# Performance work log

Measured on AMD Instinct MI355X. Metric: run time of the kernel, lower is better.

## Reference

```python
import jax, jax.numpy as jnp
import numpy as np

N = 512    # nnodes
H = 8      # attention heads
C = 32     # gnn_repr_size (per head)
ER = 32    # edge_repr_size
FE = 3     # feat_emb_size
E = 16384  # edges (avg degree 32)


def gat_conv(x, edge_index, edge_attr, W, att_src, att_dst, We, att_edge, b):
    """PyG GATConv (edge_dim=1, concat=True, add_self_loops=True, eval mode)."""
    n = x.shape[0]
    h_, c_ = att_src.shape
    row, col = edge_index[0], edge_index[1]
    # self loops with fill_value='mean': mean of incoming edge_attr per target node
    deg = jax.ops.segment_sum(jnp.ones_like(edge_attr), col, num_segments=n)
    loop_attr = jax.ops.segment_sum(edge_attr, col, num_segments=n) / jnp.maximum(deg, 1.0)
    ar = jnp.arange(n)
    row = jnp.concatenate([row, ar])
    col = jnp.concatenate([col, ar])
    ea = jnp.concatenate([edge_attr, loop_attr])
    # node projections [n, H, C]
    h = (x @ W.T).reshape(n, h_, c_)
    a_src = jnp.sum(h * att_src, axis=-1)  # [n, H]
    a_dst = jnp.sum(h * att_dst, axis=-1)  # [n, H]
    e = (ea[:, None] @ We.T).reshape(-1, h_, c_)  # [E', H, C]
    a_e = jnp.sum(e * att_edge, axis=-1)          # [E', H]
    alpha = jax.nn.leaky_relu(a_src[row] + a_dst[col] + a_e, 0.2)
    # softmax over edges grouped by destination node
    amax = jax.ops.segment_max(alpha, col, num_segments=n)
    ex = jnp.exp(alpha - amax[col])
    denom = jax.ops.segment_sum(ex, col, num_segments=n)
    alpha = ex / (denom[col] + 1e-16)
    out = jax.ops.segment_sum(h[row] * alpha[..., None], col, num_segments=n)
    return out.reshape(n, h_ * c_) + b


def setup_inputs():
    key = jax.random.key(0)
    ks = jax.random.split(key, 24)
    s = 0.05
    HC = H * C
    in_len = N * ER + 3 * N + 3 * FE  # combiner1 input length
    return {
        "dist": jax.random.uniform(ks[0], (N, N), dtype=jnp.float32),
        "markov": jax.random.uniform(ks[1], (N, N), dtype=jnp.float32),
        "demand": jax.random.normal(ks[2], (N,), dtype=jnp.float32),
        "W_week": jax.random.normal(ks[3], (7, FE)) * s,
        "W_cap": jax.random.normal(ks[4], (26, FE)) * s,
        "W_veh": jax.random.normal(ks[5], (15, FE)) * s,
        "g1_W": jax.random.normal(ks[6], (HC, 1)) * s,
        "g1_att_src": jax.random.normal(ks[7], (H, C)) * s,
        "g1_att_dst": jax.random.normal(ks[8], (H, C)) * s,
        "g1_We": jax.random.normal(ks[9], (HC, 1)) * s,
        "g1_att_edge": jax.random.normal(ks[10], (H, C)) * s,
        "g1_b": jnp.zeros((HC,), dtype=jnp.float32),
        "g2_W": jax.random.normal(ks[11], (HC, HC)) * s,
        "g2_att_src": jax.random.normal(ks[12], (H, C)) * s,
        "g2_att_dst": jax.random.normal(ks[13], (H, C)) * s,
        "g2_We": jax.random.normal(ks[14], (HC, 1)) * s,
        "g2_att_edge": jax.random.normal(ks[15], (H, C)) * s,
        "g2_b": jnp.zeros((HC,), dtype=jnp.float32),
        "Wes": jax.random.normal(ks[16], (ER, 2 * HC)) * s,
        "bes": jnp.zeros((ER,), dtype=jnp.float32),
        "Wc1": jax.random.normal(ks[17], (N, in_len)) * 0.01,
        "bc1": jnp.zeros((N,), dtype=jnp.float32),
        "Wc2": jax.random.normal(ks[18], (N, N)) * s,
        "bc2": jnp.zeros((N,), dtype=jnp.float32),
        "stops": jax.random.randint(ks[19], (256,), 0, N),
        "edge_index": jax.random.randint(ks[20], (2, E), 0, N),
        "weekday": 3,
        "vehicles": 7,
        "capacity": 12,
    }


def reference(dist, markov, demand, W_week, W_cap, W_veh,
              g1_W, g1_att_src, g1_att_dst, g1_We, g1_att_edge, g1_b,
              g2_W, g2_att_src, g2_att_dst, g2_We, g2_att_edge, g2_b,
              Wes, bes, Wc1, bc1, Wc2, bc2,
              stops, edge_index, weekday, vehicles, capacity):
    n = dist.shape[0]
    dist = (dist - dist.min()) / (dist.max() - dist.min())
    x = demand[:, None]  # [n, 1]
    ea = markov[edge_index[0], edge_index[1]]  # [E]
    x = jax.nn.relu(gat_conv(x, edge_index, ea, g1_W, g1_att_src, g1_att_dst, g1_We, g1_att_edge, g1_b))
    x = jax.nn.relu(gat_conv(x, edge_index, ea, g2_W, g2_att_src, g2_att_dst, g2_We, g2_att_edge, g2_b))
    HC_ = x.shape[1]
    # all-pairs edge representation: concat(x[i], x[j]) over meshgrid -> [n*n, 2*HC]
    er = jnp.concatenate([
        jnp.broadcast_to(x[:, None, :], (n, n, HC_)),
        jnp.broadcast_to(x[None, :, :], (n, n, HC_)),
    ], axis=-1).reshape(n * n, 2 * HC_)
    er = (er @ Wes.T + bes).reshape(n, -1)  # [n, n*ER]
    week = jnp.broadcast_to(W_week[weekday], (n, W_week.shape[1]))
    cap = jnp.broadcast_to(W_cap[capacity], (n, W_cap.shape[1]))
    veh = jnp.broadcast_to(W_veh[vehicles], (n, W_veh.shape[1]))
    stop = jnp.broadcast_to(jnp.zeros((n,), dtype=dist.dtype).at[stops].set(1.0)[None, :], (n, n))
    feat = jnp.concatenate([er, dist, markov, week, cap, veh, stop], axis=1)
    out = jax.nn.relu(feat @ Wc1.T + bc1) @ Wc2.T + bc2
    return out
```

## Files before the change

### kernel.cpp

```cpp
#include <hip/hip_runtime.h>
#include <hip/hip_bf16.h>

typedef __hip_bfloat16 bf16;
typedef __attribute__((ext_vector_type(8))) short bf16x8;
typedef __attribute__((ext_vector_type(4))) float f32x4;

#define NNODE 512
#define NEDGE 16384
#define INLEN 17929
#define K1    1056

#define WS_EA      0
#define WS_CSRC    16384
#define WS_CEA     32768
#define WS_DEG     49152
#define WS_STARTS  49664
#define WS_LATTR   50176
#define WS_MM      50688
#define WS_MMP     50690
#define WS_STOPV   50818
#define WS_AE      51330
#define WS_PS      51346
#define WS_H       55552
#define WS_G2WT    186624
#define WS_H2      317696
#define WS_ASRC    448768
#define WS_ADST    452864
#define WS_UV      456960
#define WS_K       489728
#define WS_APACK   490240
#define WS_BPACK   760576
#define WS_OUT1    1030912
#define WS_WC2B    1161984
#define WS_WESF    1293056
#define WS_ASRC2   1309440
#define WS_ADST2   1313536
#define WS_CURSOR  1317632
#define WS_DEGP    1318144
#define WS_LSUMP   1350912

__global__ __launch_bounds__(256)
void k_prep(const float* __restrict__ demand, const float* __restrict__ W1,
            const float* __restrict__ att_s, const float* __restrict__ att_d,
            const int* __restrict__ stops, const float* __restrict__ Wes,
            const float* __restrict__ dist, const float* __restrict__ markov,
            const int* __restrict__ eidx,
            const float* __restrict__ g1We, const float* __restrict__ g1ae,
            const float* __restrict__ g2We, const float* __restrict__ g2ae,
            const float* __restrict__ g2W,  const float* __restrict__ g2as,
            const float* __restrict__ g2ad, float* ws){
  int b = blockIdx.x, tid = threadIdx.x;
  if (b < 512){
    int hd = tid>>5, c = tid&31;
    float hv = demand[b] * W1[tid];
    ws[WS_H + b*256 + tid] = hv;
    float ps = hv * att_s[tid];
    float pd = hv * att_d[tid];
    for (int off=16; off; off>>=1){ ps += __shfl_down(ps,off,32); pd += __shfl_down(pd,off,32); }
    if (c==0){ ws[WS_ASRC + b*8+hd]=ps; ws[WS_ADST + b*8+hd]=pd; }
  } else if (b == 512){
    ws[WS_STOPV+tid] = 0.f; ws[WS_STOPV+256+tid] = 0.f;
    __syncthreads();
    ws[WS_STOPV + stops[tid]] = 1.0f;
    if (tid < 8){
      float s=0.f; for (int c=0;c<32;c++) s += g1We[tid*32+c]*g1ae[tid*32+c];
      ws[WS_AE+tid]=s;
    } else if (tid < 16){
      int h=tid-8; float s=0.f; for (int c=0;c<32;c++) s += g2We[h*32+c]*g2ae[h*32+c];
      ws[WS_AE+8+h]=s;
    }
  } else if (b < 515){
    for (int idx = (b-513)*8192 + tid; idx < (b-512)*8192; idx += 256){
      int k = idx>>8, c = idx&255;
      ws[WS_WESF+idx] = (k<32) ? Wes[k*512+c] : Wes[(k-32)*512+256+c];
    }
  } else if (b < 579){
    __shared__ float smn[256], smx[256];
    int p = b-515;
    float mn = 3.4e38f, mx = -3.4e38f;
    const float4* dv = (const float4*)(dist + p*4096);
    #pragma unroll
    for (int k=0;k<4;k++){
      float4 v = dv[k*256 + tid];
      mn = fminf(mn, fminf(fminf(v.x,v.y), fminf(v.z,v.w)));
      mx = fmaxf(mx, fmaxf(fmaxf(v.x,v.y), fmaxf(v.z,v.w)));
    }
    smn[tid]=mn; smx[tid]=mx; __syncthreads();
    for (int off=128; off; off>>=1){
      if (tid<off){ smn[tid]=fminf(smn[tid],smn[tid+off]); smx[tid]=fmaxf(smx[tid],smx[tid+off]); }
      __syncthreads();
    }
    if (tid==0){ ws[WS_MMP+p]=smn[0]; ws[WS_MMP+64+p]=smx[0]; }
  } else if (b < 643){
    __shared__ int   hd_[512];
    __shared__ float hf_[512];
    int k = b-579;
    hd_[tid]=0; hd_[256+tid]=0; hf_[tid]=0.f; hf_[256+tid]=0.f;
    __syncthreads();
    int e = k*256 + tid;
    int r = eidx[e], c = eidx[NEDGE+e];
    float a = markov[r*NNODE + c];
    ws[WS_EA+e] = a;
    atomicAdd(&hd_[c], 1);
    atomicAdd(&hf_[c], a);
    __syncthreads();
    ((int*)(ws+WS_DEGP))[k*512+tid]     = hd_[tid];
    ((int*)(ws+WS_DEGP))[k*512+256+tid] = hd_[256+tid];
    ws[WS_LSUMP + k*512+tid]     = hf_[tid];
    ws[WS_LSUMP + k*512+256+tid] = hf_[256+tid];
  } else if (b < 659){
    int j = b-643;
    const float* att = (j<8) ? g2as : g2ad;
    int h = j&7;
    float s = 0.f;
    for (int c=0;c<32;c++) s += att[h*32+c] * g2W[(h*32+c)*256 + tid];
    ws[WS_PS + j*256 + tid] = s;
  } else if (b < 675){
    __shared__ float T[64][65];
    int tb = b-659, tr = tb>>2, tc = tb&3;
    int w = tid>>6, c = tid&63;
    for (int k=0;k<16;k++){
      int r = k*4 + w;
      T[r][c] = g2W[(tr*64+r)*256 + tc*64 + c];
    }
    __syncthreads();
    for (int k=0;k<16;k++){
      int r = k*4 + w;
      ws[WS_G2WT + (tc*64+r)*256 + tr*64 + c] = T[c][r];
    }
  } else {
    ((int*)(ws+WS_CURSOR))[tid] = 0;
    ((int*)(ws+WS_CURSOR))[256+tid] = 0;
  }
}

__global__ __launch_bounds__(512)
void k_scansc(const int* __restrict__ eidx, float* ws){
  __shared__ int sc[512];
  __shared__ int startS[512];
  __shared__ float rmn[64], rmx[64];
  int t = threadIdx.x, b = blockIdx.x;
  const int* dp = (const int*)(ws+WS_DEGP);
  int d = 0;
  for (int k=0;k<64;k++) d += dp[k*512+t];
  sc[t] = d; __syncthreads();
  for (int off=1; off<512; off<<=1){
    int v = (t>=off) ? sc[t-off] : 0; __syncthreads();
    sc[t] += v; __syncthreads();
  }
  startS[t] = sc[t]-d;
  if (b == 0){
    float l = 0.f;
    for (int k=0;k<64;k++) l += ws[WS_LSUMP+k*512+t];
    ((int*)(ws+WS_STARTS))[t] = startS[t];
    ((int*)(ws+WS_DEG))[t] = d;
    ws[WS_LATTR+t] = l / (float)(d>1 ? d : 1);
    if (t < 64){ rmn[t]=ws[WS_MMP+t]; rmx[t]=ws[WS_MMP+64+t]; }
    __syncthreads();
    if (t == 0){
      float mn=rmn[0], mx=rmx[0];
      for (int i=1;i<64;i++){ mn=fminf(mn,rmn[i]); mx=fmaxf(mx,rmx[i]); }
      ws[WS_MM]=mn; ws[WS_MM+1]=mx;
    }
  }
  __syncthreads();
  int e = b*512 + t;
  int c = eidx[NEDGE+e];
  int p = startS[c] + atomicAdd((int*)(ws+WS_CURSOR)+c, 1);
  ((int*)(ws+WS_CSRC))[p] = eidx[e];
  ws[WS_CEA+p] = ws[WS_EA+e];
}

template<int MODE>
__global__ __launch_bounds__(256)
void k_agg(const float* __restrict__ hbuf, const float* __restrict__ asrc,
           const float* __restrict__ adst, const int* __restrict__ csrc,
           const float* __restrict__ cea, const int* __restrict__ starts,
           const int* __restrict__ deg, const float* __restrict__ lattr,
           const float* __restrict__ AEp, const float* __restrict__ bvec,
           const float* __restrict__ dist, const float* __restrict__ markov,
           float* ws){
  int t = blockIdx.x, tid = threadIdx.x, hd = tid>>5;
  __shared__ int   srcE[256];
  __shared__ float eaE[256];
  __shared__ float Lall[256*8];
  __shared__ float AE[8], mh[8], dh[8], sw[8];
  __shared__ float xrow[256], uvrow[64];
  if (tid<8) AE[tid]=AEp[tid];
  __syncthreads();
  int d = deg[t], s0 = starts[t];
  if (d > 256) d = 256;
  for (int e=tid; e<d; e+=256){ srcE[e]=csrc[s0+e]; eaE[e]=cea[s0+e]; }
  __syncthreads();
  {
    int h8 = tid&7;
    float adt = adst[t*8+h8], aeh = AE[h8];
    for (int e = tid>>3; e < d; e += 32){
      float a = asrc[srcE[e]*8+h8] + adt + eaE[e]*aeh;
      Lall[e*8+h8] = a>=0.f ? a : 0.2f*a;
    }
  }
  __syncthreads();
  {
    int h = tid>>5, j = tid&31;
    float aself = asrc[t*8+h] + adst[t*8+h] + lattr[t]*AE[h];
    aself = aself>=0.f ? aself : 0.2f*aself;
    float mm = aself;
    for (int e=j; e<d; e+=32) mm = fmaxf(mm, Lall[e*8+h]);
    for (int off=16; off; off>>=1) mm = fmaxf(mm, __shfl_down(mm,off,32));
    mm = __shfl(mm, 0, 32);
    float dd = 0.f;
    for (int e=j; e<d; e+=32) dd += __expf(Lall[e*8+h]-mm);
    for (int off=16; off; off>>=1) dd += __shfl_down(dd,off,32);
    if (j==0){
      float se = __expf(aself-mm);
      mh[h]=mm; dh[h]=dd+se+1e-16f; sw[h]=se;
    }
  }
  __syncthreads();
  {
    int h8 = tid&7;
    for (int e = tid>>3; e < d; e += 32)
      Lall[e*8+h8] = __expf(Lall[e*8+h8] - mh[h8]);
  }
  __syncthreads();
  float a0 = sw[hd]*hbuf[t*256+tid], a1=0.f, a2=0.f, a3=0.f;
  int e = 0;
  for (; e+4<=d; e+=4){
    a0 += Lall[(e+0)*8+hd]*hbuf[srcE[e+0]*256+tid];
    a1 += Lall[(e+1)*8+hd]*hbuf[srcE[e+1]*256+tid];
    a2 += Lall[(e+2)*8+hd]*hbuf[srcE[e+2]*256+tid];
    a3 += Lall[(e+3)*8+hd]*hbuf[srcE[e+3]*256+tid];
  }
  for (; e<d; e++) a0 += Lall[e*8+hd]*hbuf[srcE[e]*256+tid];
  float v = fmaxf(((a0+a1)+(a2+a3))/dh[hd] + bvec[tid], 0.f);
  xrow[tid] = v;
  __syncthreads();
  if (MODE == 1){
    const float* g2wt = ws + WS_G2WT;
    float h0=0.f,h1=0.f,h2=0.f,h3=0.f;
    for (int c=0;c<256;c+=4){
      h0 += xrow[c+0]*g2wt[(c+0)*256+tid];
      h1 += xrow[c+1]*g2wt[(c+1)*256+tid];
      h2 += xrow[c+2]*g2wt[(c+2)*256+tid];
      h3 += xrow[c+3]*g2wt[(c+3)*256+tid];
    }
    ws[WS_H2 + t*256 + tid] = (h0+h1)+(h2+h3);
    if (tid < 64){
      int j = tid>>2, q = tid&3;
      const float* pr = ws + WS_PS + j*256 + q*64;
      const float* xr = xrow + q*64;
      float p = 0.f;
      for (int c=0;c<64;c++) p += xr[c]*pr[c];
      p += __shfl_down(p,2,4);
      p += __shfl_down(p,1,4);
      if (q==0){
        if (j<8) ws[WS_ASRC2 + t*8+j] = p;
        else     ws[WS_ADST2 + t*8+(j-8)] = p;
      }
    }
  } else {
    int k = tid>>2, q = tid&3;
    const float* wr = ws + WS_WESF + k*256 + q*64;
    const float* xr = xrow + q*64;
    float p = 0.f;
    for (int c=0;c<64;c++) p += xr[c]*wr[c];
    p += __shfl_down(p,2,4);
    p += __shfl_down(p,1,4);
    if (q==0){ ws[WS_UV + t*64+k] = p; uvrow[k] = p; }
    __syncthreads();
    float mn = ws[WS_MM], mx = ws[WS_MM+1];
    float inv = 1.0f/(mx-mn);
    bf16* ap = (bf16*)(ws+WS_APACK);
    const float* mrow = markov + t*512;
    for (int j=tid; j<K1; j+=256){
      float v2;
      if (j<32)       v2 = uvrow[j];
      else if (j<544) v2 = (dist[t*512 + j-32] - mn) * inv;
      else            v2 = mrow[j-544];
      ap[(size_t)t*K1 + j] = __float2bfloat16(v2);
    }
  }
}

__global__ __launch_bounds__(1024)
void k_skpack(const float* __restrict__ Wc1, const float* __restrict__ bc1,
              const float* __restrict__ bes, const float* __restrict__ Wweek,
              const float* __restrict__ Wcap, const float* __restrict__ Wveh,
              const int* __restrict__ wd, const int* __restrict__ vh,
              const int* __restrict__ cp, const float* __restrict__ Wc2,
              float* ws){
  int o = blockIdx.x, tid = threadIdx.x;
  __shared__ float besf[32];
  __shared__ float red[1024];
  if (tid<32) besf[tid] = bes[tid];
  __syncthreads();
  const float* wr = Wc1 + (size_t)o*INLEN;
  bf16* bp  = (bf16*)(ws+WS_BPACK);
  bf16* w2b = (bf16*)(ws+WS_WC2B);
  float be = besf[tid&31];
  const float* uvp = ws + WS_UV + ((tid>>5)<<6) + 32 + (tid&31);
  float sP = 0.f, tP0=0.f, tP1=0.f, tP2=0.f, tP3=0.f;
  #pragma unroll
  for (int i=0;i<16;i+=4){
    float w0 = wr[tid + 1024*(i+0)];
    float w1 = wr[tid + 1024*(i+1)];
    float w2 = wr[tid + 1024*(i+2)];
    float w3 = wr[tid + 1024*(i+3)];
    float u0 = uvp[2048*(i+0)];
    float u1 = uvp[2048*(i+1)];
    float u2 = uvp[2048*(i+2)];
    float u3 = uvp[2048*(i+3)];
    sP += (w0+w1)+(w2+w3);
    tP0 += w0*(u0+be);
    tP1 += w1*(u1+be);
    tP2 += w2*(u2+be);
    tP3 += w3*(u3+be);
  }
  float tP = (tP0+tP1)+(tP2+tP3);
  if (tid < 512) tP += ws[WS_STOPV+tid] * wr[17417+tid];
  if (tid < 9){
    int g = tid/3, f = tid-g*3;
    float sv = (g==0) ? Wweek[wd[0]*3+f]
             : (g==1) ? Wcap[cp[0]*3+f]
                      : Wveh[vh[0]*3+f];
    tP += sv * wr[17408+tid];
  }
  red[tid] = sP; __syncthreads();
  for (int off=512; off>=32; off>>=1){
    if (tid<off) red[tid] += red[tid+off];
    __syncthreads();
  }
  if (tid<32) bp[(size_t)o*K1 + tid] = __float2bfloat16(red[tid]);
  __syncthreads();
  red[tid] = tP; __syncthreads();
  for (int off=512; off; off>>=1){
    if (tid<off) red[tid] += red[tid+off];
    __syncthreads();
  }
  if (tid==0) ws[WS_K+o] = red[0] + bc1[o];
  bp[(size_t)o*K1 + 32 + tid] = __float2bfloat16(wr[16384+tid]);
  if (tid < 512) w2b[o*512+tid] = __float2bfloat16(Wc2[o*512+tid]);
}

template<bool RELU, bool BF16OUT>
__global__ __launch_bounds__(256)
void gemm_mfma(const bf16* __restrict__ A, const bf16* __restrict__ B,
               const float* __restrict__ bias, float* __restrict__ Cf,
               bf16* __restrict__ Cb, int M, int N, int K){
  __shared__ short Als[2][2048];
  __shared__ short Bls[2][2048];
  const int tid = threadIdx.x;
  const int bm = blockIdx.y*64, bn = blockIdx.x*64;
  const int wave = tid>>6, lane = tid&63;
  const int wm = wave>>1, wn = wave&1;
  const int r = lane&15, q = lane>>4;
  f32x4 acc[2][2] = {};
  const int lrow = tid>>2, lq = tid&3;
  const bf16* Ag = A + (size_t)(bm+lrow)*K + lq*8;
  const bf16* Bg = B + (size_t)(bn+lrow)*K + lq*8;
  const int sidx = (lq*64+lrow)*8;
  const int nk = K>>5;
  float4 av = *(const float4*)(Ag);
  float4 bv = *(const float4*)(Bg);
  *(float4*)(&Als[0][sidx]) = av;
  *(float4*)(&Bls[0][sidx]) = bv;
  __syncthreads();
  for (int kk=0; kk<nk; kk++){
    int cur = kk&1, nxt = cur^1;
    if (kk+1 < nk){
      av = *(const float4*)(Ag + (kk+1)*32);
      bv = *(const float4*)(Bg + (kk+1)*32);
    }
    #pragma unroll
    for (int i=0;i<2;i++){
      bf16x8 af = *(const bf16x8*)(&Als[cur][(q*64 + wm*32 + i*16 + r)*8]);
      #pragma unroll
      for (int j=0;j<2;j++){
        bf16x8 bfr = *(const bf16x8*)(&Bls[cur][(q*64 + wn*32 + j*16 + r)*8]);
        acc[i][j] = __builtin_amdgcn_mfma_f32_16x16x32_bf16(af, bfr, acc[i][j], 0,0,0);
      }
    }
    if (kk+1 < nk){
      __syncthreads();
      *(float4*)(&Als[nxt][sidx]) = av;
      *(float4*)(&Bls[nxt][sidx]) = bv;
      __syncthreads();
    }
  }
  #pragma unroll
  for (int i=0;i<2;i++){
    int row = bm + wm*32 + i*16 + q*4;
    #pragma unroll
    for (int j=0;j<2;j++){
      int col = bn + wn*32 + j*16 + r;
      float bi = bias ? bias[col] : 0.f;
      #pragma unroll
      for (int g=0; g<4; g++){
        float v = acc[i][j][g] + bi;
        if (RELU) v = fmaxf(v, 0.f);
        if (BF16OUT) Cb[(size_t)(row+g)*N + col] = __float2bfloat16(v);
        else         Cf[(size_t)(row+g)*N + col] = v;
      }
    }
  }
}

extern "C" void kernel_launch(void* const* d_in, const int* in_sizes, int n_in,
                              void* d_out, int out_size, void* d_ws, size_t ws_size,
                              hipStream_t stream){
  const float* dist   = (const float*)d_in[0];
  const float* markov = (const float*)d_in[1];
  const float* demand = (const float*)d_in[2];
  const float* Wweek  = (const float*)d_in[3];
  const float* Wcap   = (const float*)d_in[4];
  const float* Wveh   = (const float*)d_in[5];
  const float* g1W    = (const float*)d_in[6];
  const float* g1as   = (const float*)d_in[7];
  const float* g1ad   = (const float*)d_in[8];
  const float* g1We   = (const float*)d_in[9];
  const float* g1ae   = (const float*)d_in[10];
  const float* g1b    = (const float*)d_in[11];
  const float* g2W    = (const float*)d_in[12];
  const float* g2as   = (const float*)d_in[13];
  const float* g2ad   = (const float*)d_in[14];
  const float* g2We   = (const float*)d_in[15];
  const float* g2ae   = (const float*)d_in[16];
  const float* g2b    = (const float*)d_in[17];
  const float* Wes    = (const float*)d_in[18];
  const float* bes    = (const float*)d_in[19];
  const float* Wc1    = (const float*)d_in[20];
  const float* bc1    = (const float*)d_in[21];
  const float* Wc2    = (const float*)d_in[22];
  const float* bc2    = (const float*)d_in[23];
  const int*   stops  = (const int*)d_in[24];
  const int*   eidx   = (const int*)d_in[25];
  const int*   wd     = (const int*)d_in[26];
  const int*   vh     = (const int*)d_in[27];
  const int*   cp     = (const int*)d_in[28];
  float* out = (float*)d_out;
  float* ws = (float*)d_ws;

  const int*   csrc   = (const int*)(ws+WS_CSRC);
  const float* cea    = ws+WS_CEA;
  const int*   starts = (const int*)(ws+WS_STARTS);
  const int*   deg    = (const int*)(ws+WS_DEG);
  const float* lattr  = ws+WS_LATTR;

  k_prep<<<676,256,0,stream>>>(demand, g1W, g1as, g1ad, stops, Wes, dist, markov, eidx,
                               g1We, g1ae, g2We, g2ae, g2W, g2as, g2ad, ws);
  k_scansc<<<32,512,0,stream>>>(eidx, ws);
  k_agg<1><<<512,256,0,stream>>>(ws+WS_H, ws+WS_ASRC, ws+WS_ADST, csrc, cea, starts, deg,
                                 lattr, ws+WS_AE, g1b, dist, markov, ws);
  k_agg<2><<<512,256,0,stream>>>(ws+WS_H2, ws+WS_ASRC2, ws+WS_ADST2, csrc, cea, starts, deg,
                                 lattr, ws+WS_AE+8, g2b, dist, markov, ws);
  k_skpack<<<512,1024,0,stream>>>(Wc1, bc1, bes, Wweek, Wcap, Wveh, wd, vh, cp, Wc2, ws);
  gemm_mfma<true,true><<<dim3(8,8),256,0,stream>>>((const bf16*)(ws+WS_APACK), (const bf16*)(ws+WS_BPACK),
                                                   ws+WS_K, nullptr, (bf16*)(ws+WS_OUT1), 512, 512, K1);
  gemm_mfma<false,false><<<dim3(8,8),256,0,stream>>>((const bf16*)(ws+WS_OUT1), (const bf16*)(ws+WS_WC2B),
                                                     bc2, out, nullptr, 512, 512, 512);
}
```

Measured before the change: 204.8 us.

## Widen GEMM to 512 threads with K=64 steps, shuffle reductions, move Wc2 cast

The MFMA GEMM now runs 8 waves per 64x64 tile with a 64-wide K step, so each wave owns a 32x16 output and there are half as many barriers per K. To fit the wider step, the first GEMM's K is zero-padded from 1056 to 1088. The k_skpack reductions switch from shared-memory trees with many barriers to wave shuffles plus a small final pass. The Wc2 bf16 conversion moves into extra k_prep blocks using vectorised loads and stores. The trade-off is more shared memory per block and some padded zero work.

```diff
diff --git a/kernel.cpp b/kernel.cpp
--- a/kernel.cpp
+++ b/kernel.cpp
@@ -8,7 +8,7 @@
 #define NNODE 512
 #define NEDGE 16384
 #define INLEN 17929
-#define K1    1056
+#define K1P   1088
 
 #define WS_EA      0
 #define WS_CSRC    16384
@@ -29,15 +29,20 @@
 #define WS_UV      456960
 #define WS_K       489728
 #define WS_APACK   490240
-#define WS_BPACK   760576
-#define WS_OUT1    1030912
-#define WS_WC2B    1161984
-#define WS_WESF    1293056
-#define WS_ASRC2   1309440
-#define WS_ADST2   1313536
-#define WS_CURSOR  1317632
-#define WS_DEGP    1318144
-#define WS_LSUMP   1350912
+#define WS_BPACK   768768
+#define WS_OUT1    1047296
+#define WS_WC2B    1178368
+#define WS_WESF    1309440
+#define WS_ASRC2   1325824
+#define WS_ADST2   1329920
+#define WS_CURSOR  1334016
+#define WS_DEGP    1334528
+#define WS_LSUMP   1367296
+
+static __device__ __forceinline__ unsigned short f2bfbits(float x){
+  bf16 b = __float2bfloat16(x);
+  union { bf16 b; unsigned short u; } c; c.b = b; return c.u;
+}
 
 __global__ __launch_bounds__(256)
 void k_prep(const float* __restrict__ demand, const float* __restrict__ W1,
@@ -48,7 +53,8 @@
             const float* __restrict__ g1We, const float* __restrict__ g1ae,
             const float* __restrict__ g2We, const float* __restrict__ g2ae,
             const float* __restrict__ g2W,  const float* __restrict__ g2as,
-            const float* __restrict__ g2ad, float* ws){
+            const float* __restrict__ g2ad, const float* __restrict__ Wc2,
+            float* ws){
   int b = blockIdx.x, tid = threadIdx.x;
   if (b < 512){
     int hd = tid>>5, c = tid&31;
@@ -128,9 +134,21 @@
       int r = k*4 + w;
       ws[WS_G2WT + (tc*64+r)*256 + tr*64 + c] = T[c][r];
     }
-  } else {
+  } else if (b == 675){
     ((int*)(ws+WS_CURSOR))[tid] = 0;
     ((int*)(ws+WS_CURSOR))[256+tid] = 0;
+  } else {
+    int blk = b - 676;
+    const float4* src = (const float4*)(Wc2 + blk*4096);
+    ushort4* dst = (ushort4*)((unsigned short*)(ws+WS_WC2B) + blk*4096);
+    #pragma unroll
+    for (int i=0;i<4;i++){
+      float4 v = src[i*256+tid];
+      ushort4 u;
+      u.x = f2bfbits(v.x); u.y = f2bfbits(v.y);
+      u.z = f2bfbits(v.z); u.w = f2bfbits(v.w);
+      dst[i*256+tid] = u;
+    }
   }
 }
 
@@ -273,12 +291,13 @@
     float inv = 1.0f/(mx-mn);
     bf16* ap = (bf16*)(ws+WS_APACK);
     const float* mrow = markov + t*512;
-    for (int j=tid; j<K1; j+=256){
+    for (int j=tid; j<K1P; j+=256){
       float v2;
-      if (j<32)       v2 = uvrow[j];
-      else if (j<544) v2 = (dist[t*512 + j-32] - mn) * inv;
-      else            v2 = mrow[j-544];
-      ap[(size_t)t*K1 + j] = __float2bfloat16(v2);
+      if (j<32)        v2 = uvrow[j];
+      else if (j<544)  v2 = (dist[t*512 + j-32] - mn) * inv;
+      else if (j<1056) v2 = mrow[j-544];
+      else             v2 = 0.f;
+      ap[(size_t)t*K1P + j] = __float2bfloat16(v2);
     }
   }
 }
@@ -288,16 +307,15 @@
               const float* __restrict__ bes, const float* __restrict__ Wweek,
               const float* __restrict__ Wcap, const float* __restrict__ Wveh,
               const int* __restrict__ wd, const int* __restrict__ vh,
-              const int* __restrict__ cp, const float* __restrict__ Wc2,
-              float* ws){
+              const int* __restrict__ cp, float* ws){
   int o = blockIdx.x, tid = threadIdx.x;
   __shared__ float besf[32];
-  __shared__ float red[1024];
+  __shared__ float red[512];
+  __shared__ float red2[16];
   if (tid<32) besf[tid] = bes[tid];
   __syncthreads();
   const float* wr = Wc1 + (size_t)o*INLEN;
   bf16* bp  = (bf16*)(ws+WS_BPACK);
-  bf16* w2b = (bf16*)(ws+WS_WC2B);
   float be = besf[tid&31];
   const float* uvp = ws + WS_UV + ((tid>>5)<<6) + 32 + (tid&31);
   float sP = 0.f, tP0=0.f, tP1=0.f, tP2=0.f, tP3=0.f;
@@ -326,41 +344,45 @@
                       : Wveh[vh[0]*3+f];
     tP += sv * wr[17408+tid];
   }
-  red[tid] = sP; __syncthreads();
-  for (int off=512; off>=32; off>>=1){
-    if (tid<off) red[tid] += red[tid+off];
-    __syncthreads();
-  }
-  if (tid<32) bp[(size_t)o*K1 + tid] = __float2bfloat16(red[tid]);
-  __syncthreads();
-  red[tid] = tP; __syncthreads();
-  for (int off=512; off; off>>=1){
-    if (tid<off) red[tid] += red[tid+off];
-    __syncthreads();
-  }
-  if (tid==0) ws[WS_K+o] = red[0] + bc1[o];
-  bp[(size_t)o*K1 + 32 + tid] = __float2bfloat16(wr[16384+tid]);
-  if (tid < 512) w2b[o*512+tid] = __float2bfloat16(Wc2[o*512+tid]);
+  int lane = tid&63, w = tid>>6;
+  sP += __shfl_down(sP, 32, 64);
+  if (lane < 32) red[w*32 + lane] = sP;
+  for (int off=32; off; off>>=1) tP += __shfl_down(tP, off, 64);
+  if (lane == 0) red2[w] = tP;
+  __syncthreads();
+  if (tid < 32){
+    float s = 0.f;
+    #pragma unroll
+    for (int k=0;k<16;k++) s += red[k*32+tid];
+    bp[(size_t)o*K1P + tid] = __float2bfloat16(s);
+    bp[(size_t)o*K1P + 1056 + tid] = __float2bfloat16(0.f);
+  } else if (tid == 32){
+    float s = 0.f;
+    #pragma unroll
+    for (int k=0;k<16;k++) s += red2[k];
+    ws[WS_K+o] = s + bc1[o];
+  }
+  bp[(size_t)o*K1P + 32 + tid] = __float2bfloat16(wr[16384+tid]);
 }
 
 template<bool RELU, bool BF16OUT>
-__global__ __launch_bounds__(256)
+__global__ __launch_bounds__(512)
 void gemm_mfma(const bf16* __restrict__ A, const bf16* __restrict__ B,
                const float* __restrict__ bias, float* __restrict__ Cf,
                bf16* __restrict__ Cb, int M, int N, int K){
-  __shared__ short Als[2][2048];
-  __shared__ short Bls[2][2048];
+  __shared__ short Als[2][4096];
+  __shared__ short Bls[2][4096];
   const int tid = threadIdx.x;
   const int bm = blockIdx.y*64, bn = blockIdx.x*64;
   const int wave = tid>>6, lane = tid&63;
-  const int wm = wave>>1, wn = wave&1;
+  const int wm = wave>>2, wn = wave&3;
   const int r = lane&15, q = lane>>4;
-  f32x4 acc[2][2] = {};
-  const int lrow = tid>>2, lq = tid&3;
-  const bf16* Ag = A + (size_t)(bm+lrow)*K + lq*8;
-  const bf16* Bg = B + (size_t)(bn+lrow)*K + lq*8;
-  const int sidx = (lq*64+lrow)*8;
-  const int nk = K>>5;
+  f32x4 acc[2] = {};
+  const int lrow = tid>>3, lk8 = tid&7;
+  const bf16* Ag = A + (size_t)(bm+lrow)*K + lk8*8;
+  const bf16* Bg = B + (size_t)(bn+lrow)*K + lk8*8;
+  const int sidx = ((lk8>>2)*256 + (lk8&3)*64 + lrow)*8;
+  const int nk = K>>6;
   float4 av = *(const float4*)(Ag);
   float4 bv = *(const float4*)(Bg);
   *(float4*)(&Als[0][sidx]) = av;
@@ -369,16 +391,16 @@
   for (int kk=0; kk<nk; kk++){
     int cur = kk&1, nxt = cur^1;
     if (kk+1 < nk){
-      av = *(const float4*)(Ag + (kk+1)*32);
-      bv = *(const float4*)(Bg + (kk+1)*32);
-    }
-    #pragma unroll
-    for (int i=0;i<2;i++){
-      bf16x8 af = *(const bf16x8*)(&Als[cur][(q*64 + wm*32 + i*16 + r)*8]);
+      av = *(const float4*)(Ag + (kk+1)*64);
+      bv = *(const float4*)(Bg + (kk+1)*64);
+    }
+    #pragma unroll
+    for (int kk2=0; kk2<2; kk2++){
+      bf16x8 bfr = *(const bf16x8*)(&Bls[cur][(kk2*256 + q*64 + wn*16 + r)*8]);
       #pragma unroll
-      for (int j=0;j<2;j++){
-        bf16x8 bfr = *(const bf16x8*)(&Bls[cur][(q*64 + wn*32 + j*16 + r)*8]);
-        acc[i][j] = __builtin_amdgcn_mfma_f32_16x16x32_bf16(af, bfr, acc[i][j], 0,0,0);
+      for (int i=0;i<2;i++){
+        bf16x8 af = *(const bf16x8*)(&Als[cur][(kk2*256 + q*64 + wm*32 + i*16 + r)*8]);
+        acc[i] = __builtin_amdgcn_mfma_f32_16x16x32_bf16(af, bfr, acc[i], 0,0,0);
       }
     }
     if (kk+1 < nk){
@@ -391,17 +413,14 @@
   #pragma unroll
   for (int i=0;i<2;i++){
     int row = bm + wm*32 + i*16 + q*4;
-    #pragma unroll
-    for (int j=0;j<2;j++){
-      int col = bn + wn*32 + j*16 + r;
-      float bi = bias ? bias[col] : 0.f;
-      #pragma unroll
-      for (int g=0; g<4; g++){
-        float v = acc[i][j][g] + bi;
-        if (RELU) v = fmaxf(v, 0.f);
-        if (BF16OUT) Cb[(size_t)(row+g)*N + col] = __float2bfloat16(v);
-        else         Cf[(size_t)(row+g)*N + col] = v;
-      }
+    int col = bn + wn*16 + r;
+    float bi = bias ? bias[col] : 0.f;
+    #pragma unroll
+    for (int g=0; g<4; g++){
+      float v = acc[i][g] + bi;
+      if (RELU) v = fmaxf(v, 0.f);
+      if (BF16OUT) Cb[(size_t)(row+g)*N + col] = __float2bfloat16(v);
+      else         Cf[(size_t)(row+g)*N + col] = v;
     }
   }
 }
@@ -447,16 +466,16 @@
   const int*   deg    = (const int*)(ws+WS_DEG);
   const float* lattr  = ws+WS_LATTR;
 
-  k_prep<<<676,256,0,stream>>>(demand, g1W, g1as, g1ad, stops, Wes, dist, markov, eidx,
-                               g1We, g1ae, g2We, g2ae, g2W, g2as, g2ad, ws);
+  k_prep<<<740,256,0,stream>>>(demand, g1W, g1as, g1ad, stops, Wes, dist, markov, eidx,
+                               g1We, g1ae, g2We, g2ae, g2W, g2as, g2ad, Wc2, ws);
   k_scansc<<<32,512,0,stream>>>(eidx, ws);
   k_agg<1><<<512,256,0,stream>>>(ws+WS_H, ws+WS_ASRC, ws+WS_ADST, csrc, cea, starts, deg,
                                  lattr, ws+WS_AE, g1b, dist, markov, ws);
   k_agg<2><<<512,256,0,stream>>>(ws+WS_H2, ws+WS_ASRC2, ws+WS_ADST2, csrc, cea, starts, deg,
                                  lattr, ws+WS_AE+8, g2b, dist, markov, ws);
-  k_skpack<<<512,1024,0,stream>>>(Wc1, bc1, bes, Wweek, Wcap, Wveh, wd, vh, cp, Wc2, ws);
-  gemm_mfma<true,true><<<dim3(8,8),256,0,stream>>>((const bf16*)(ws+WS_APACK), (const bf16*)(ws+WS_BPACK),
-                                                   ws+WS_K, nullptr, (bf16*)(ws+WS_OUT1), 512, 512, K1);
-  gemm_mfma<false,false><<<dim3(8,8),256,0,stream>>>((const bf16*)(ws+WS_OUT1), (const bf16*)(ws+WS_WC2B),
+  k_skpack<<<512,1024,0,stream>>>(Wc1, bc1, bes, Wweek, Wcap, Wveh, wd, vh, cp, ws);
+  gemm_mfma<true,true><<<dim3(8,8),512,0,stream>>>((const bf16*)(ws+WS_APACK), (const bf16*)(ws+WS_BPACK),
+                                                   ws+WS_K, nullptr, (bf16*)(ws+WS_OUT1), 512, 512, K1P);
+  gemm_mfma<false,false><<<dim3(8,8),512,0,stream>>>((const bf16*)(ws+WS_OUT1), (const bf16*)(ws+WS_WC2B),
                                                      bc2, out, nullptr, 512, 512, 512);
 }
```

Measured after the change: 204.4 us. About the same (-0.2%).
